# Kernel tuning notes

Measured on AMD Instinct MI355X. Metric: run time of the kernel, lower is better.

Reference implementation:

```python
import jax, jax.numpy as jnp
import numpy as np

VOCAB = 256
EMB = 128
HID = 512
OUT = 256
B = 64
L = 1024


def setup_inputs() -> dict:
    key = jax.random.key(0)
    ks = jax.random.split(key, 6)
    x = jax.random.randint(ks[0], (B, L), 0, VOCAB, dtype=jnp.int32)
    hidden = jnp.zeros((B, HID), dtype=jnp.float32)
    embedding = jax.random.normal(ks[1], (VOCAB, EMB), dtype=jnp.float32)
    W_e = jax.random.normal(ks[2], (EMB, HID), dtype=jnp.float32) * 0.01
    W_h = jax.random.normal(ks[3], (HID, HID), dtype=jnp.float32) * 0.01
    b_h = jnp.zeros((1, HID), dtype=jnp.float32)
    W_o = jax.random.normal(ks[4], (HID, OUT), dtype=jnp.float32) * 0.01
    b_o = jnp.zeros((OUT,), dtype=jnp.float32)
    return {"x": x, "hidden": hidden, "embedding": embedding, "W_e": W_e,
            "W_h": W_h, "b_h": b_h, "W_o": W_o, "b_o": b_o}


def reference(x, hidden, embedding, W_e, W_h, b_h, W_o, b_o):
    # x: [b, l] int ids -> embed: [l, b, emb] (time-major for the scan)
    x_embed = embedding[x]                      # [b, l, emb]
    x_embed = jnp.swapaxes(x_embed, 0, 1)       # [l, b, emb]
    # Precompute input projection for all timesteps (same math, batched):
    hx_all = jnp.einsum('lbe,eh->lbh', x_embed, W_e)  # [l, b, hid]

    def step(h_prev, hx_t):
        h_t = jnp.tanh(hx_t + h_prev @ W_h + b_h)
        return h_t, h_t

    final_hidden, outputs = jax.lax.scan(step, hidden, hx_all)  # outputs: [l, b, hid]
    outputs = jnp.swapaxes(outputs, 0, 1)                        # [b, l, hid]
    logits = outputs @ W_o + b_o                                  # [b, l, out]
    return logits, final_hidden
```

## Files before the change

### kernel.cpp

```cpp
#include <hip/hip_runtime.h>

typedef float f32x4 __attribute__((ext_vector_type(4)));
typedef int   i32x4 __attribute__((ext_vector_type(4)));
typedef short s16x8 __attribute__((ext_vector_type(8)));

#define VOCAB 256
#define EMB   128
#define HID   512
#define OUT_D 256
#define BATCH 64
#define SEQ   1024

__device__ __forceinline__ unsigned short f2bf(float f) {
  unsigned u = __builtin_bit_cast(unsigned, f);
  u += 0x7fffu + ((u >> 16) & 1u);
  return (unsigned short)(u >> 16);
}

__global__ void k_e2(const float* __restrict__ emb, const float* __restrict__ We,
                     const float* __restrict__ bh, float* __restrict__ E2)
{
  __shared__ float el[EMB];
  const int v = blockIdx.x, c = threadIdx.x;
  if (c < EMB) el[c] = emb[v * EMB + c];
  __syncthreads();
  float s = bh[c];
  #pragma unroll
  for (int e = 0; e < EMB; ++e) s += el[e] * We[e * HID + c];
  E2[v * HID + c] = s;
}

__global__ void k_whfrag(const float* __restrict__ Wh, i32x4* __restrict__ WhF)
{
  const int g = blockIdx.x * 256 + threadIdx.x;
  const int lane = g & 63, frag = g >> 6;
  const int kt = frag & 7, ct = frag >> 3;
  const int col = (ct << 4) + (lane & 15);
  const int kb  = (kt << 6) + ((lane >> 4) << 4);
  int wd[4];
  #pragma unroll
  for (int q = 0; q < 4; ++q) {
    int b[4];
    #pragma unroll
    for (int j = 0; j < 4; ++j) {
      float s = Wh[(kb + q * 4 + j) * HID + col] * 2048.f;
      s = fminf(fmaxf(s, -127.f), 127.f);
      b[j] = __float2int_rn(s) & 255;
    }
    wd[q] = b[0] | (b[1] << 8) | (b[2] << 16) | (b[3] << 24);
  }
  i32x4 v = {wd[0], wd[1], wd[2], wd[3]};
  WhF[g] = v;
}

__global__ void k_wot(const float* __restrict__ Wo, unsigned short* __restrict__ WoT)
{
  const int k = blockIdx.x;
  const int c = threadIdx.x;
  WoT[c * HID + k] = f2bf(Wo[k * OUT_D + c] * (1.0f / 127.0f));
}

__global__ __launch_bounds__(1024, 4) void k_scan(
    const int* __restrict__ x, const float* __restrict__ h0,
    const float* __restrict__ E2, const i32x4* __restrict__ WhF,
    char* __restrict__ hist, float* __restrict__ fh)
{
  __shared__ __align__(16) char hbuf[2][HID];
  const int tid  = threadIdx.x;
  const int wv   = tid >> 6, lane = tid & 63;
  const int lrow = lane & 15, lhi = lane >> 4;
  const int row  = blockIdx.x;
  const int col  = (wv << 5) + ((lhi & 1) << 4) + lrow;

  i32x4 bfr[2][8];
  #pragma unroll
  for (int nt = 0; nt < 2; ++nt)
    #pragma unroll
    for (int kt = 0; kt < 8; ++kt)
      bfr[nt][kt] = WhF[((((wv << 1) + nt) << 3) + kt) * 64 + lane];

  if (tid < HID) {
    float s = fminf(fmaxf(h0[(row << 9) + tid] * 127.f, -127.f), 127.f);
    hbuf[0][tid] = (char)__float2int_rn(s);
  }

  const int id0 = x[(row << 10) + 0];
  int idA = x[(row << 10) + 1], idB;
  float hxA = E2[(id0 << 9) + col], hxB;
  __syncthreads();

  const float inv = 1.f / (127.f * 2048.f);
  const float TC  = 2.8853900817779268f;

#define STEP(T, PH, HXU, HXP, IDU, IDL)                                       \
  {                                                                           \
    const int t_ = (T);                                                       \
           \
    i32x4 fv;                                                                 \
    if (tid < 32) fv = *(const i32x4*)(&hbuf[PH][tid << 4]);                  \
                 \
    HXP = E2[((IDU) << 9) + col];                                             \
                                               \
    IDL = x[(row << 10) + ((t_ + 2 > SEQ - 1) ? SEQ - 1 : t_ + 2)];           \
      \
    i32x4 acc[2] = {};                                                        \
    _Pragma("unroll") for (int kt = 0; kt < 8; ++kt) {                        \
      i32x4 a = *(const i32x4*)(&hbuf[PH][(kt << 6) + (lhi << 4)]);           \
      _Pragma("unroll") for (int nt = 0; nt < 2; ++nt)                        \
        acc[nt] = __builtin_amdgcn_mfma_i32_16x16x64_i8(a, bfr[nt][kt],       \
                                                        acc[nt], 0, 0, 0);    \
    }                                                                         \
                     \
    if (t_ > 0 && tid < 32)                                                   \
      __builtin_nontemporal_store(fv, (i32x4*)(hist +                         \
          (((size_t)(row << 10) + (t_ - 1)) << 10) + (tid << 4)));            \
                   \
    int av = (lhi & 1) ? acc[1][0] : acc[0][0];                               \
                              \
    float z = fmaf((float)av, inv, HXU);                                      \
    float e = __builtin_amdgcn_exp2f(z * TC);                                 \
    float h = fmaf(-2.f, __builtin_amdgcn_rcpf(1.f + e), 1.f);                \
    hbuf[1 - (PH)][col] = (char)__float2int_rn(h * 127.f);                    \
    if (t_ == SEQ - 1) fh[(row << 9) + col] = h;                              \
    asm volatile("s_waitcnt lgkmcnt(0)" ::: "memory");                        \
    __builtin_amdgcn_sched_barrier(0);                                        \
    __builtin_amdgcn_s_barrier();                                             \
    __builtin_amdgcn_sched_barrier(0);                                        \
  }

  for (int T2 = 0; T2 < SEQ / 2; ++T2) {
    STEP(2 * T2,     0, hxA, hxB, idA, idB)
    STEP(2 * T2 + 1, 1, hxB, hxA, idB, idA)
  }
#undef STEP

  if (tid < 32) {
    i32x4 fv = *(const i32x4*)(&hbuf[0][tid << 4]);
    __builtin_nontemporal_store(fv, (i32x4*)(hist +
        (((size_t)(row << 10) + (SEQ - 1)) << 10) + (tid << 4)));
  }
}

__global__ __launch_bounds__(256) void k_logits(const char* __restrict__ hist,
                                                const unsigned short* __restrict__ WoT,
                                                const float* __restrict__ bo, float* out)
{
  __shared__ __align__(16) char As[64 * 1024];
  const int tid = threadIdx.x;
  const int m0 = blockIdx.x * 64;

  for (int i = tid; i < 1024; i += 256) {
    const int row = i >> 4, seg = i & 15;
    const char* src = hist + (size_t)(m0 + row) * 1024 + seg * 32;
    i32x4 w0 = *(const i32x4*)(src);
    i32x4 w1 = *(const i32x4*)(src + 16);
    unsigned od[16];
    #pragma unroll
    for (int d = 0; d < 8; ++d) {
      const unsigned dw = (unsigned)(d < 4 ? w0[d] : w1[d - 4]);
      const int q0 = (int)(signed char)(dw & 0xffu);
      const int q1 = (int)(signed char)((dw >> 8) & 0xffu);
      const int q2 = (int)(signed char)((dw >> 16) & 0xffu);
      const int q3 = (int)(signed char)(dw >> 24);
      const unsigned u0 = __builtin_bit_cast(unsigned, (float)q0);
      const unsigned u1 = __builtin_bit_cast(unsigned, (float)q1);
      const unsigned u2 = __builtin_bit_cast(unsigned, (float)q2);
      const unsigned u3 = __builtin_bit_cast(unsigned, (float)q3);
      od[2 * d]     = (u0 >> 16) | (u1 & 0xffff0000u);
      od[2 * d + 1] = (u2 >> 16) | (u3 & 0xffff0000u);
    }
    #pragma unroll
    for (int q = 0; q < 4; ++q) {
      i32x4 v = {(int)od[4 * q], (int)od[4 * q + 1],
                 (int)od[4 * q + 2], (int)od[4 * q + 3]};
      const int off = seg * 64 + q * 16;
      *(i32x4*)(&As[row * 1024 + (off ^ ((row & 7) << 4))]) = v;
    }
  }
  __syncthreads();

  const int wv = tid >> 6, lane = tid & 63, lrow = lane & 15, lhi = lane >> 4;
  const int cb = wv << 6;
  f32x4 acc[4][4] = {};
  #pragma unroll
  for (int kt = 0; kt < 16; ++kt) {
    s16x8 a[4], b[4];
    #pragma unroll
    for (int mt = 0; mt < 4; ++mt) {
      const int row = mt * 16 + lrow;
      a[mt] = *(const s16x8*)(&As[row * 1024 + ((kt * 64 + lhi * 16) ^ ((row & 7) << 4))]);
    }
    #pragma unroll
    for (int nt = 0; nt < 4; ++nt) {
      const int col = cb + nt * 16 + lrow;
      b[nt] = *(const s16x8*)((const char*)WoT + col * 1024 + kt * 64 + lhi * 16);
    }
    #pragma unroll
    for (int mt = 0; mt < 4; ++mt)
      #pragma unroll
      for (int nt = 0; nt < 4; ++nt)
        acc[mt][nt] = __builtin_amdgcn_mfma_f32_16x16x32_bf16(a[mt], b[nt], acc[mt][nt], 0, 0, 0);
  }
  #pragma unroll
  for (int nt = 0; nt < 4; ++nt) {
    const float bb = bo[cb + nt * 16 + lrow];
    #pragma unroll
    for (int mt = 0; mt < 4; ++mt)
      #pragma unroll
      for (int r = 0; r < 4; ++r)
        out[(size_t)(m0 + mt * 16 + lhi * 4 + r) * OUT_D + cb + nt * 16 + lrow] =
            acc[mt][nt][r] + bb;
  }
}

extern "C" void kernel_launch(void* const* d_in, const int* in_sizes, int n_in,
                              void* d_out, int out_size, void* d_ws, size_t ws_size,
                              hipStream_t stream)
{
  const int*   x   = (const int*)  d_in[0];
  const float* h0  = (const float*)d_in[1];
  const float* emb = (const float*)d_in[2];
  const float* We  = (const float*)d_in[3];
  const float* Wh  = (const float*)d_in[4];
  const float* bh  = (const float*)d_in[5];
  const float* Wo  = (const float*)d_in[6];
  const float* bo  = (const float*)d_in[7];
  float* out = (float*)d_out;
  char*  ws  = (char*)d_ws;

  float*          E2  = (float*)ws;
  i32x4*          WhF = (i32x4*)(ws + (512 << 10));
  unsigned short* WoT = (unsigned short*)(ws + (768 << 10));

  k_e2    <<<VOCAB, HID,   0, stream>>>(emb, We, bh, E2);
  k_whfrag<<<64,    256,   0, stream>>>(Wh, WhF);
  k_wot   <<<HID,   OUT_D, 0, stream>>>(Wo, WoT);

  k_scan  <<<BATCH, 1024, 0, stream>>>(x, h0, E2, WhF,
                                       (char*)d_out,
                                       out + (size_t)BATCH * SEQ * OUT_D);
  k_logits<<<(BATCH * SEQ) / 64, 256, 0, stream>>>(
      (const char*)d_out, WoT, bo, out);
}
```

Measured before the change: 728.2 us.

## Split each batch row's recurrence across two workgroups exchanging hidden halves via global flags

```diff
diff --git a/kernel.cpp b/kernel.cpp
--- a/kernel.cpp
+++ b/kernel.cpp
@@ -60,26 +60,38 @@
   WoT[c * HID + k] = f2bf(Wo[k * OUT_D + c] * (1.0f / 127.0f));
 }
 
-__global__ __launch_bounds__(1024, 4) void k_scan(
+__global__ __launch_bounds__(512, 2) void k_scan(
     const int* __restrict__ x, const float* __restrict__ h0,
     const float* __restrict__ E2, const i32x4* __restrict__ WhF,
+    unsigned int* __restrict__ xb,
     char* __restrict__ hist, float* __restrict__ fh)
 {
   __shared__ __align__(16) char hbuf[2][HID];
   const int tid  = threadIdx.x;
   const int wv   = tid >> 6, lane = tid & 63;
   const int lrow = lane & 15, lhi = lane >> 4;
-  const int row  = blockIdx.x;
-  const int col  = (wv << 5) + ((lhi & 1) << 4) + lrow;
+  const int b    = blockIdx.x;
+  const int row  = b & 63, H = b >> 6;
+  const int colL = (wv << 5) + ((lhi & 1) << 4) + lrow;
+  const int col  = (H << 8) + colL;
 
   i32x4 bfr[2][8];
   #pragma unroll
   for (int nt = 0; nt < 2; ++nt)
     #pragma unroll
     for (int kt = 0; kt < 8; ++kt)
-      bfr[nt][kt] = WhF[((((wv << 1) + nt) << 3) + kt) * 64 + lane];
-
-  if (tid < HID) {
+      bfr[nt][kt] = WhF[(((H << 4) + (wv << 1) + nt) * 8 + kt) * 64 + lane];
+
+  const int hbL = (H << 8) + (lhi << 4);
+  const int hbR = ((1 - H) << 8) + (lhi << 4);
+  const int pubLds = (H << 8) + (wv << 5) + (lane << 1);
+  unsigned int* const xb_my = xb + (((row << 1) + H) << 8);
+  unsigned int* const xb_pt = xb + (((row << 1) + (1 - H)) << 8);
+  const int conLds = ((1 - H) << 8) + (lane << 1);
+  const int histLds = (H << 8) + (lane << 4);
+  char* const histG = hist + ((size_t)row << 20) + (H << 8) + (lane << 4);
+
+  {
     float s = fminf(fmaxf(h0[(row << 9) + tid] * 127.f, -127.f), 127.f);
     hbuf[0][tid] = (char)__float2int_rn(s);
   }
@@ -95,33 +107,67 @@
 #define STEP(T, PH, HXU, HXP, IDU, IDL)                                       \
   {                                                                           \
     const int t_ = (T);                                                       \
-           \
-    i32x4 fv;                                                                 \
-    if (tid < 32) fv = *(const i32x4*)(&hbuf[PH][tid << 4]);                  \
-                 \
+              \
+    i32x4 fvh;                                                                \
+    if (wv == 3 && lane < 16) fvh = *(const i32x4*)(&hbuf[PH][histLds]);      \
+                          \
     HXP = E2[((IDU) << 9) + col];                                             \
-                                               \
     IDL = x[(row << 10) + ((t_ + 2 > SEQ - 1) ? SEQ - 1 : t_ + 2)];           \
-      \
+                    \
     i32x4 acc[2] = {};                                                        \
-    _Pragma("unroll") for (int kt = 0; kt < 8; ++kt) {                        \
-      i32x4 a = *(const i32x4*)(&hbuf[PH][(kt << 6) + (lhi << 4)]);           \
-      _Pragma("unroll") for (int nt = 0; nt < 2; ++nt)                        \
-        acc[nt] = __builtin_amdgcn_mfma_i32_16x16x64_i8(a, bfr[nt][kt],       \
-                                                        acc[nt], 0, 0, 0);    \
-    }                                                                         \
-                     \
-    if (t_ > 0 && tid < 32)                                                   \
-      __builtin_nontemporal_store(fv, (i32x4*)(hist +                         \
-          (((size_t)(row << 10) + (t_ - 1)) << 10) + (tid << 4)));            \
-                   \
+    _Pragma("unroll") for (int k4 = 0; k4 < 4; ++k4) {                        \
+      i32x4 a = *(const i32x4*)(&hbuf[PH][hbL + (k4 << 6)]);                  \
+      const int kt = (H << 2) + k4;                                           \
+      acc[0] = __builtin_amdgcn_mfma_i32_16x16x64_i8(a, bfr[0][kt], acc[0], 0, 0, 0); \
+      acc[1] = __builtin_amdgcn_mfma_i32_16x16x64_i8(a, bfr[1][kt], acc[1], 0, 0, 0); \
+    }                                                                         \
+              \
+    if (t_ > 0) {                                                             \
+      if (wv == 1) {                                                          \
+        const unsigned int* src = xb_pt + ((t_ & 1) << 7);                    \
+        unsigned int d0, d1;                                                  \
+        const unsigned tag = (unsigned)t_;                                    \
+        for (;;) {                                                            \
+          d0 = __hip_atomic_load(src + lane,      __ATOMIC_RELAXED,           \
+                                 __HIP_MEMORY_SCOPE_AGENT);                   \
+          d1 = __hip_atomic_load(src + 64 + lane, __ATOMIC_RELAXED,           \
+                                 __HIP_MEMORY_SCOPE_AGENT);                   \
+          if (__all(((d0 >> 16) == tag) & ((d1 >> 16) == tag))) break;        \
+        }                                                                     \
+        *(unsigned short*)(&hbuf[PH][conLds])       = (unsigned short)d0;     \
+        *(unsigned short*)(&hbuf[PH][conLds + 128]) = (unsigned short)d1;     \
+      }                                                                       \
+      asm volatile("s_waitcnt lgkmcnt(0)" ::: "memory");                      \
+      __builtin_amdgcn_sched_barrier(0);                                      \
+      __builtin_amdgcn_s_barrier();                                           \
+      __builtin_amdgcn_sched_barrier(0);                                      \
+    }                                                                         \
+                                                      \
+    _Pragma("unroll") for (int k4 = 0; k4 < 4; ++k4) {                        \
+      i32x4 a = *(const i32x4*)(&hbuf[PH][hbR + (k4 << 6)]);                  \
+      const int kt = ((1 - H) << 2) + k4;                                     \
+      acc[0] = __builtin_amdgcn_mfma_i32_16x16x64_i8(a, bfr[0][kt], acc[0], 0, 0, 0); \
+      acc[1] = __builtin_amdgcn_mfma_i32_16x16x64_i8(a, bfr[1][kt], acc[1], 0, 0, 0); \
+    }                                                                         \
+              \
+    if (t_ > 0 && wv == 3 && lane < 16)                                       \
+      __builtin_nontemporal_store(fvh,                                        \
+          (i32x4*)(histG + ((unsigned)(t_ - 1) << 10)));                      \
+                             \
     int av = (lhi & 1) ? acc[1][0] : acc[0][0];                               \
-                              \
     float z = fmaf((float)av, inv, HXU);                                      \
     float e = __builtin_amdgcn_exp2f(z * TC);                                 \
     float h = fmaf(-2.f, __builtin_amdgcn_rcpf(1.f + e), 1.f);                \
     hbuf[1 - (PH)][col] = (char)__float2int_rn(h * 127.f);                    \
     if (t_ == SEQ - 1) fh[(row << 9) + col] = h;                              \
+       \
+    asm volatile("s_waitcnt lgkmcnt(0)" ::: "memory");                        \
+    if (lane < 16) {                                                          \
+      unsigned v16 = *(const unsigned short*)(&hbuf[1 - (PH)][pubLds]);       \
+      unsigned dw = v16 | ((unsigned)(t_ + 1) << 16);                         \
+      __hip_atomic_store(xb_my + (((t_ + 1) & 1) << 7) + (wv << 4) + lane,    \
+                         dw, __ATOMIC_RELAXED, __HIP_MEMORY_SCOPE_AGENT);     \
+    }                                                                         \
     asm volatile("s_waitcnt lgkmcnt(0)" ::: "memory");                        \
     __builtin_amdgcn_sched_barrier(0);                                        \
     __builtin_amdgcn_s_barrier();                                             \
@@ -134,10 +180,9 @@
   }
 #undef STEP
 
-  if (tid < 32) {
-    i32x4 fv = *(const i32x4*)(&hbuf[0][tid << 4]);
-    __builtin_nontemporal_store(fv, (i32x4*)(hist +
-        (((size_t)(row << 10) + (SEQ - 1)) << 10) + (tid << 4)));
+  if (wv == 3 && lane < 16) {
+    i32x4 fvh = *(const i32x4*)(&hbuf[0][histLds]);
+    __builtin_nontemporal_store(fvh, (i32x4*)(histG + ((unsigned)(SEQ - 1) << 10)));
   }
 }
 
@@ -231,14 +276,17 @@
   float*          E2  = (float*)ws;
   i32x4*          WhF = (i32x4*)(ws + (512 << 10));
   unsigned short* WoT = (unsigned short*)(ws + (768 << 10));
+  unsigned int*   xb  = (unsigned int*)(ws + (1024 << 10));
+
+  hipMemsetAsync(xb, 0, 128 << 10, stream);
 
   k_e2    <<<VOCAB, HID,   0, stream>>>(emb, We, bh, E2);
   k_whfrag<<<64,    256,   0, stream>>>(Wh, WhF);
   k_wot   <<<HID,   OUT_D, 0, stream>>>(Wo, WoT);
 
-  k_scan  <<<BATCH, 1024, 0, stream>>>(x, h0, E2, WhF,
-                                       (char*)d_out,
-                                       out + (size_t)BATCH * SEQ * OUT_D);
+  k_scan  <<<2 * BATCH, 512, 0, stream>>>(x, h0, E2, WhF, xb,
+                                          (char*)d_out,
+                                          out + (size_t)BATCH * SEQ * OUT_D);
   k_logits<<<(BATCH * SEQ) / 64, 256, 0, stream>>>(
       (const char*)d_out, WoT, bo, out);
 }
```

Result: slower. 2.542 ms (+249.0%).
